# Optimization experiments

Measured on AMD Instinct MI355X. Metric: run time of the kernel, lower is better.

Reference implementation:

```python
import jax, jax.numpy as jnp
import numpy as np

NUM_EXPERTS = 16
TOP_K = 2


def setup_inputs() -> dict:
    key = jax.random.key(0)
    k1, k2, k3 = jax.random.split(key, 3)
    T, H, V = 2048, 2048, 32000
    hidden_states = jax.random.normal(k1, (T, H), dtype=jnp.float32)
    gate_w = jax.random.normal(k2, (NUM_EXPERTS, H), dtype=jnp.float32) * 0.02
    expert_biases = jax.random.normal(k3, (NUM_EXPERTS, V), dtype=jnp.float32) * 0.02
    return {"hidden_states": hidden_states, "gate_w": gate_w, "expert_biases": expert_biases}


def reference(hidden_states, gate_w, expert_biases):
    # gate logits: (T, E)
    gate_logits = jnp.einsum("th,eh->te", hidden_states, gate_w)
    gate_scores = jax.nn.softmax(gate_logits, axis=-1)
    topk_scores, topk_indices = jax.lax.top_k(gate_scores, TOP_K)  # (T, K)
    topk_scores = topk_scores / jnp.sum(topk_scores, axis=-1, keepdims=True)
    # gather expert bias rows: (T, K, V), then weighted sum over K -> (T, V)
    gathered = jnp.take(expert_biases, topk_indices, axis=0)
    bias = jnp.einsum("tk,tkv->tv", topk_scores, gathered)
    # load-balancing aux loss
    expert_usage = jnp.mean(gate_scores, axis=0)  # (E,)
    aux_loss = jnp.sum(expert_usage * jnp.log(expert_usage)) * NUM_EXPERTS
    return bias, aux_loss
```

## Files before the change

kernel.cpp:

```cpp
#include <hip/hip_runtime.h>
#include <math.h>

#define T_TOK 2048
#define H_DIM 2048
#define V_DIM 32000
#define NE    16

__global__ __launch_bounds__(256) void gate_kernel(const float* __restrict__ hs,
                                                   const float* __restrict__ gw,
                                                   float* __restrict__ usage,
                                                   float4* __restrict__ params)
{
    const int t   = blockIdx.x;
    const int tid = threadIdx.x;

    float acc[NE];
#pragma unroll
    for (int e = 0; e < NE; ++e) acc[e] = 0.f;

    const float* hrow = hs + (size_t)t * H_DIM;
#pragma unroll
    for (int i = tid; i < H_DIM; i += 256) {
        float x = hrow[i];
#pragma unroll
        for (int e = 0; e < NE; ++e) acc[e] += x * gw[e * H_DIM + i];
    }

#pragma unroll
    for (int e = 0; e < NE; ++e) {
        float v = acc[e];
#pragma unroll
        for (int off = 32; off > 0; off >>= 1) v += __shfl_down(v, off, 64);
        acc[e] = v;
    }

    __shared__ float partial[4][NE];
    __shared__ float logits[NE];
    __shared__ float exps[NE + 1];

    const int wave = tid >> 6, lane = tid & 63;
    if (lane == 0) {
#pragma unroll
        for (int e = 0; e < NE; ++e) partial[wave][e] = acc[e];
    }
    __syncthreads();

    if (tid < NE)
        logits[tid] = partial[0][tid] + partial[1][tid] + partial[2][tid] + partial[3][tid];
    __syncthreads();

    if (tid == 0) {
        float m = logits[0];
#pragma unroll
        for (int e = 1; e < NE; ++e) m = fmaxf(m, logits[e]);
        float Z = 0.f;
#pragma unroll
        for (int e = 0; e < NE; ++e) { float ex = expf(logits[e] - m); exps[e] = ex; Z += ex; }
        exps[NE] = Z;

        int i0 = 0; float l0 = logits[0];
#pragma unroll
        for (int e = 1; e < NE; ++e) if (logits[e] > l0) { l0 = logits[e]; i0 = e; }
        int i1 = -1; float l1 = -INFINITY;
#pragma unroll
        for (int e = 0; e < NE; ++e) if (e != i0 && logits[e] > l1) { l1 = logits[e]; i1 = e; }

        float e0 = exps[i0], e1 = exps[i1];
        float inv = 1.f / (e0 + e1);
        params[t] = make_float4(e0 * inv, e1 * inv, __int_as_float(i0), __int_as_float(i1));
    }
    __syncthreads();

    if (tid < NE)
        atomicAdd(usage + tid, exps[tid] / exps[NE]);
}

__global__ __launch_bounds__(256) void bias_kernel(const float4* __restrict__ eb,
                                                   const float4* __restrict__ params,
                                                   float4* __restrict__ out)
{
    const int V4 = V_DIM / 4;
    unsigned int n = blockIdx.x * 256u + threadIdx.x;
    int t = (int)(n / (unsigned)V4);
    int v = (int)(n % (unsigned)V4);

    float4 p = params[t];
    int i0 = __float_as_int(p.z), i1 = __float_as_int(p.w);

    float4 a = eb[(size_t)i0 * V4 + v];
    float4 b = eb[(size_t)i1 * V4 + v];
    float4 r;
    r.x = p.x * a.x + p.y * b.x;
    r.y = p.x * a.y + p.y * b.y;
    r.z = p.x * a.z + p.y * b.z;
    r.w = p.x * a.w + p.y * b.w;
    out[n] = r;
}

__global__ void aux_kernel(const float* __restrict__ usage, float* __restrict__ out)
{
    int tid = threadIdx.x;
    float v = 0.f;
    if (tid < NE) {
        float u = usage[tid] / (float)T_TOK;
        v = u * logf(u);
    }
#pragma unroll
    for (int off = 8; off > 0; off >>= 1) v += __shfl_down(v, off, 64);
    if (tid == 0) out[0] = v * (float)NE;
}

extern "C" void kernel_launch(void* const* d_in, const int* in_sizes, int n_in,
                              void* d_out, int out_size, void* d_ws, size_t ws_size,
                              hipStream_t stream)
{
    const float* hs = (const float*)d_in[0];
    const float* gw = (const float*)d_in[1];
    const float* eb = (const float*)d_in[2];
    float* out = (float*)d_out;

    float*  usage  = (float*)d_ws;
    float4* params = (float4*)((char*)d_ws + 256);

    hipMemsetAsync(d_ws, 0, 256, stream);

    gate_kernel<<<T_TOK, 256, 0, stream>>>(hs, gw, usage, params);

    const unsigned total4 = (unsigned)T_TOK * (V_DIM / 4);
    bias_kernel<<<total4 / 256, 256, 0, stream>>>((const float4*)eb, params, (float4*)out);

    aux_kernel<<<1, 64, 0, stream>>>(usage, out + (size_t)T_TOK * V_DIM);
}
```

Measured before the change: 312.6 us.

## Vectorize gate loads, replace usage atomics with score buffer, nontemporal bias stores

The gate kernel now reads hidden states and gate weights as float4. Per-token softmax scores are written to a workspace buffer instead of being atomically added into a shared usage array, which also removes the memset. A 1024-thread aux kernel reduces that buffer deterministically. The bias kernel writes its large output with nontemporal stores to avoid polluting cache. The cost is an extra 128KB workspace write and read.

```diff
diff --git a/kernel.cpp b/kernel.cpp
--- a/kernel.cpp
+++ b/kernel.cpp
@@ -6,24 +6,33 @@
 #define V_DIM 32000
 #define NE    16
 
-__global__ __launch_bounds__(256) void gate_kernel(const float* __restrict__ hs,
-                                                   const float* __restrict__ gw,
-                                                   float* __restrict__ usage,
+typedef float fvec4 __attribute__((ext_vector_type(4)));
+
+#define WS_SCORES(ws)  ((float*)(ws))
+#define WS_PARAMS(ws)  ((float4*)((char*)(ws) + NE * T_TOK * sizeof(float)))
+
+__global__ __launch_bounds__(256) void gate_kernel(const float4* __restrict__ hs,
+                                                   const float4* __restrict__ gw,
+                                                   float* __restrict__ scores,
                                                    float4* __restrict__ params)
 {
     const int t   = blockIdx.x;
     const int tid = threadIdx.x;
+    const int H4  = H_DIM / 4;
 
     float acc[NE];
 #pragma unroll
     for (int e = 0; e < NE; ++e) acc[e] = 0.f;
 
-    const float* hrow = hs + (size_t)t * H_DIM;
+    const float4* hrow = hs + (size_t)t * H4;
 #pragma unroll
-    for (int i = tid; i < H_DIM; i += 256) {
-        float x = hrow[i];
+    for (int i = tid; i < H4; i += 256) {
+        float4 x = hrow[i];
 #pragma unroll
-        for (int e = 0; e < NE; ++e) acc[e] += x * gw[e * H_DIM + i];
+        for (int e = 0; e < NE; ++e) {
+            float4 g = gw[e * H4 + i];
+            acc[e] += x.x * g.x + x.y * g.y + x.z * g.z + x.w * g.w;
+        }
     }
 
 #pragma unroll
@@ -35,7 +44,6 @@
     }
 
     __shared__ float partial[4][NE];
-    __shared__ float logits[NE];
     __shared__ float exps[NE + 1];
 
     const int wave = tid >> 6, lane = tid & 63;
@@ -45,14 +53,14 @@
     }
     __syncthreads();
 
-    if (tid < NE)
-        logits[tid] = partial[0][tid] + partial[1][tid] + partial[2][tid] + partial[3][tid];
-    __syncthreads();
-
     if (tid == 0) {
-        float m = logits[0];
+        float logits[NE];
+        float m = -INFINITY;
 #pragma unroll
-        for (int e = 1; e < NE; ++e) m = fmaxf(m, logits[e]);
+        for (int e = 0; e < NE; ++e) {
+            logits[e] = partial[0][e] + partial[1][e] + partial[2][e] + partial[3][e];
+            m = fmaxf(m, logits[e]);
+        }
         float Z = 0.f;
 #pragma unroll
         for (int e = 0; e < NE; ++e) { float ex = expf(logits[e] - m); exps[e] = ex; Z += ex; }
@@ -72,7 +80,7 @@
     __syncthreads();
 
     if (tid < NE)
-        atomicAdd(usage + tid, exps[tid] / exps[NE]);
+        scores[tid * T_TOK + t] = exps[tid] / exps[NE];
 }
 
 __global__ __launch_bounds__(256) void bias_kernel(const float4* __restrict__ eb,
@@ -89,25 +97,40 @@
 
     float4 a = eb[(size_t)i0 * V4 + v];
     float4 b = eb[(size_t)i1 * V4 + v];
-    float4 r;
+    fvec4 r;
     r.x = p.x * a.x + p.y * b.x;
     r.y = p.x * a.y + p.y * b.y;
     r.z = p.x * a.z + p.y * b.z;
     r.w = p.x * a.w + p.y * b.w;
-    out[n] = r;
+    __builtin_nontemporal_store(r, (fvec4*)out + n);
 }
 
-__global__ void aux_kernel(const float* __restrict__ usage, float* __restrict__ out)
+__global__ __launch_bounds__(1024) void aux_kernel(const float* __restrict__ scores,
+                                                   float* __restrict__ out)
 {
-    int tid = threadIdx.x;
-    float v = 0.f;
-    if (tid < NE) {
-        float u = usage[tid] / (float)T_TOK;
-        v = u * logf(u);
+    const int e    = threadIdx.x >> 6;
+    const int lane = threadIdx.x & 63;
+
+    float s = 0.f;
+    const float* row = scores + e * T_TOK;
+#pragma unroll
+    for (int i = lane; i < T_TOK; i += 64) s += row[i];
+#pragma unroll
+    for (int off = 32; off > 0; off >>= 1) s += __shfl_down(s, off, 64);
+
+    __shared__ float u[NE];
+    if (lane == 0) u[e] = s;
+    __syncthreads();
+
+    if (threadIdx.x == 0) {
+        float aux = 0.f;
+#pragma unroll
+        for (int i = 0; i < NE; ++i) {
+            float ui = u[i] / (float)T_TOK;
+            aux += ui * logf(ui);
+        }
+        out[0] = aux * (float)NE;
     }
-#pragma unroll
-    for (int off = 8; off > 0; off >>= 1) v += __shfl_down(v, off, 64);
-    if (tid == 0) out[0] = v * (float)NE;
 }
 
 extern "C" void kernel_launch(void* const* d_in, const int* in_sizes, int n_in,
@@ -119,15 +142,14 @@
     const float* eb = (const float*)d_in[2];
     float* out = (float*)d_out;
 
-    float*  usage  = (float*)d_ws;
-    float4* params = (float4*)((char*)d_ws + 256);
+    float*  scores = WS_SCORES(d_ws);
+    float4* params = WS_PARAMS(d_ws);
 
-    hipMemsetAsync(d_ws, 0, 256, stream);
-
-    gate_kernel<<<T_TOK, 256, 0, stream>>>(hs, gw, usage, params);
+    gate_kernel<<<T_TOK, 256, 0, stream>>>((const float4*)hs, (const float4*)gw,
+                                           scores, params);
 
     const unsigned total4 = (unsigned)T_TOK * (V_DIM / 4);
     bias_kernel<<<total4 / 256, 256, 0, stream>>>((const float4*)eb, params, (float4*)out);
 
-    aux_kernel<<<1, 64, 0, stream>>>(usage, out + (size_t)T_TOK * V_DIM);
+    aux_kernel<<<1, 1024, 0, stream>>>(scores, out + (size_t)T_TOK * V_DIM);
 }
```

Result: faster. 294.1 us (-5.9%).
